# Kernel optimization log

Measured on AMD Instinct MI355X. Metric: run time of the kernel, lower is better.

The kernel has to match this reference:

```python
import jax, jax.numpy as jnp
import numpy as np

B, C, C2, E = 4, 1024, 1024, 1024
D = 1024          # context_size (d_q = d_kv)
NH = 16           # module's n_heads arg -> actual head_dim after the quirky view
G = D // NH       # effective number of head groups = 64


def setup_inputs() -> dict:
    key = jax.random.key(0)
    ks = jax.random.split(key, 6)
    s = 0.02
    return {
        "x1": jax.random.normal(ks[0], (B, C, E), dtype=jnp.float32),
        "x2": jax.random.normal(ks[1], (B, C2, E), dtype=jnp.float32),
        "W_q": jax.random.normal(ks[2], (E, D), dtype=jnp.float32) * s,
        "W_k": jax.random.normal(ks[3], (E, D), dtype=jnp.float32) * s,
        "W_v": jax.random.normal(ks[4], (E, D), dtype=jnp.float32) * s,
        "W_o": jax.random.normal(ks[5], (D, D), dtype=jnp.float32) * s,
    }


def _split_heads(t):
    # (B, S, D) -> view (B, S, G, NH) -> transpose(1,2) -> (B, G, S, NH)
    b, s, _ = t.shape
    return jnp.transpose(t.reshape(b, s, G, NH), (0, 2, 1, 3))


def reference(x1, x2, W_q, W_k, W_v, W_o):
    Q = _split_heads(x1 @ W_q)   # (B, G, C, NH)
    K = _split_heads(x2 @ W_k)   # (B, G, C2, NH)
    V = _split_heads(x2 @ W_v)   # (B, G, C2, NH)
    scale = 1.0 / jnp.sqrt(jnp.asarray(NH, dtype=Q.dtype))
    scores = jnp.einsum("bgqh,bgkh->bgqk", Q, K) * scale  # (B, G, C, C2)
    w = jax.nn.softmax(scores, axis=-1)
    out = jnp.einsum("bgqk,bgkh->bgqh", w, V)             # (B, G, C, NH)
    out = jnp.transpose(out, (0, 2, 1, 3)).reshape(B, C, D)
    return out @ W_o  # dropout p=0 -> identity
```

## Files before the change

kernel.cpp:

```cpp
#include <hip/hip_runtime.h>


typedef _Float16 f16x8 __attribute__((ext_vector_type(8)));
typedef _Float16 f16x4 __attribute__((ext_vector_type(4)));
typedef _Float16 f16x2 __attribute__((ext_vector_type(2)));
typedef float    f32x4 __attribute__((ext_vector_type(4)));

#define GLOAD_LDS16(gp, lp)                                              \
    __builtin_amdgcn_global_load_lds(                                    \
        (const __attribute__((address_space(1))) void*)(gp),             \
        (__attribute__((address_space(3))) void*)(lp), 16, 0, 0)

static __device__ __forceinline__ f16x4 pack4(f32x4 p) {
    f16x2 a = __builtin_bit_cast(f16x2, __builtin_amdgcn_cvt_pkrtz(p[0], p[1]));
    f16x2 b = __builtin_bit_cast(f16x2, __builtin_amdgcn_cvt_pkrtz(p[2], p[3]));
    f16x4 r; r[0] = a[0]; r[1] = a[1]; r[2] = b[0]; r[3] = b[1];
    return r;
}

__global__ __launch_bounds__(256) void cvt2_kernel(const float* __restrict__ x1,
                                                   const float* __restrict__ x2,
                                                   _Float16* __restrict__ y1,
                                                   _Float16* __restrict__ y2) {
    int i = blockIdx.x * 256 + threadIdx.x;
    const float* x = (i < 1048576) ? x1 : x2;
    _Float16* y = (i < 1048576) ? y1 : y2;
    int j = i & 1048575;
    float4 v = ((const float4*)x)[j];
    f16x4 h = { (_Float16)v.x, (_Float16)v.y, (_Float16)v.z, (_Float16)v.w };
    ((f16x4*)y)[j] = h;
}

__global__ __launch_bounds__(256) void transpose_cvt4_kernel(
        const float* __restrict__ W0, const float* __restrict__ W1,
        const float* __restrict__ W2, const float* __restrict__ W3,
        _Float16* __restrict__ T0, _Float16* __restrict__ T1,
        _Float16* __restrict__ T2, _Float16* __restrict__ T3) {
    int z = blockIdx.z;
    const float* W = (z == 0) ? W0 : (z == 1) ? W1 : (z == 2) ? W2 : W3;
    _Float16* WT = (z == 0) ? T0 : (z == 1) ? T1 : (z == 2) ? T2 : T3;
    __shared__ float tile[32][33];
    int tx = threadIdx.x, ty = threadIdx.y;
    int c0 = blockIdx.x * 32, r0 = blockIdx.y * 32;
#pragma unroll
    for (int i = 0; i < 32; i += 8)
        tile[ty + i][tx] = W[(r0 + ty + i) * 1024 + (c0 + tx)];
    __syncthreads();
#pragma unroll
    for (int i = 0; i < 32; i += 8)
        WT[(c0 + ty + i) * 1024 + (r0 + tx)] = (_Float16)tile[tx][ty + i];
}

template <bool OUTF32>
static __device__ __forceinline__ void gemm_body(const _Float16* __restrict__ A,
                                                 const _Float16* __restrict__ BT,
                                                 void* __restrict__ Cout,
                                                 _Float16* As, _Float16* Bs) {
    const int tid = threadIdx.x, lane = tid & 63, wave = tid >> 6;
    const int wm = wave >> 1, wn = wave & 1;
    const int col = lane & 15, quad = lane >> 4;
    const int m0 = blockIdx.y * 128, n0 = blockIdx.x * 128;

    f32x4 acc[4][4];
#pragma unroll
    for (int i = 0; i < 4; i++)
#pragma unroll
        for (int j = 0; j < 4; j++) acc[i][j] = (f32x4){0.f, 0.f, 0.f, 0.f};

    const int srow = wave * 8 + (lane >> 3);
    const int sch = (lane & 7) * 8;
    const _Float16* Ag = A + (size_t)(m0 + srow) * 1024 + sch;
    const _Float16* Bg = BT + (size_t)(n0 + srow) * 1024 + sch;
    _Float16* Asl = As + wave * 512;
    _Float16* Bsl = Bs + wave * 512;

    for (int kt = 0; kt < 16; kt++) {
        __syncthreads();
#pragma unroll
        for (int c = 0; c < 4; c++) {
            GLOAD_LDS16(Ag + (size_t)(c * 32) * 1024 + kt * 64, Asl + c * 2048);
            GLOAD_LDS16(Bg + (size_t)(c * 32) * 1024 + kt * 64, Bsl + c * 2048);
        }
        __syncthreads();
#pragma unroll
        for (int ki = 0; ki < 2; ki++) {
            f16x8 af[4], bf[4];
#pragma unroll
            for (int i = 0; i < 4; i++)
                af[i] = *(const f16x8*)(As + (wm * 64 + i * 16 + col) * 64 + ki * 32 + quad * 8);
#pragma unroll
            for (int j = 0; j < 4; j++)
                bf[j] = *(const f16x8*)(Bs + (wn * 64 + j * 16 + col) * 64 + ki * 32 + quad * 8);
#pragma unroll
            for (int i = 0; i < 4; i++)
#pragma unroll
                for (int j = 0; j < 4; j++)
                    acc[i][j] = __builtin_amdgcn_mfma_f32_16x16x32_f16(af[i], bf[j], acc[i][j], 0, 0, 0);
        }
    }

#pragma unroll
    for (int i = 0; i < 4; i++)
#pragma unroll
        for (int ii = 0; ii < 4; ii++) {
            int row = m0 + wm * 64 + i * 16 + quad * 4 + ii;
#pragma unroll
            for (int j = 0; j < 4; j++) {
                int cc = n0 + wn * 64 + j * 16 + col;
                if (OUTF32) ((float*)Cout)[(size_t)row * 1024 + cc] = acc[i][j][ii];
                else ((_Float16*)Cout)[(size_t)row * 1024 + cc] = (_Float16)acc[i][j][ii];
            }
        }
}

__global__ __launch_bounds__(256, 3) void gemm_qkv_kernel(
        const _Float16* __restrict__ x1h, const _Float16* __restrict__ x2h,
        const _Float16* __restrict__ WqT, const _Float16* __restrict__ WkT,
        const _Float16* __restrict__ WvT,
        _Float16* __restrict__ Qh, _Float16* __restrict__ Kh, _Float16* __restrict__ Vh) {
    __shared__ _Float16 As[128 * 64], Bs[128 * 64];
    int z = blockIdx.z;
    const _Float16* A = (z == 0) ? x1h : x2h;
    const _Float16* BT = (z == 0) ? WqT : (z == 1) ? WkT : WvT;
    _Float16* C = (z == 0) ? Qh : (z == 1) ? Kh : Vh;
    gemm_body<false>(A, BT, (void*)C, As, Bs);
}

__global__ __launch_bounds__(256, 3) void gemm_wo_kernel(const _Float16* __restrict__ Ah,
                                                         const _Float16* __restrict__ WoT,
                                                         float* __restrict__ out) {
    __shared__ _Float16 As[128 * 64], Bs[128 * 64];
    gemm_body<true>(Ah, WoT, (void*)out, As, Bs);
}

__global__ __launch_bounds__(512, 4) void attn_kernel(const _Float16* __restrict__ Qh,
                                                      const _Float16* __restrict__ Kh,
                                                      const _Float16* __restrict__ Vh,
                                                      _Float16* __restrict__ Ah) {
    int pair = blockIdx.y;
    int b = pair >> 6, g = pair & 63;
    extern __shared__ _Float16 smem[];
    _Float16* Ks = smem;
    _Float16* Vts = smem + 16384;

    const _Float16* Kg = Kh + (size_t)(b * 1024) * 1024 + g * 16;
    const _Float16* Vg = Vh + (size_t)(b * 1024) * 1024 + g * 16;
    int tid = threadIdx.x;
#pragma unroll
    for (int it = 0; it < 4; it++) {
        int row = it * 256 + (tid >> 1);
        int part = (tid & 1) * 8;
        *(uint4*)(Ks + row * 16 + part) = *(const uint4*)(Kg + (size_t)row * 1024 + part);
    }
#pragma unroll
    for (int it = 0; it < 4; it++) {
        int row = it * 256 + (tid >> 1);
        int part = (tid & 1) * 8;
        f16x8 v = *(const f16x8*)(Vg + (size_t)row * 1024 + part);
#pragma unroll
        for (int j = 0; j < 8; j++) {
            int h = part + j;
            Vts[h * 1024 + ((row + 68 * h) & 1023)] = v[j];
        }
    }
    __syncthreads();

    int lane = tid & 63, wave = tid >> 6;
    int col = lane & 15, quad = lane >> 4;
    int q0 = blockIdx.x * 512 + wave * 64;

    f16x4 qf[4];
    const _Float16* qb = Qh + (size_t)(b * 1024 + q0 + col) * 1024 + g * 16 + quad * 4;
#pragma unroll
    for (int qg = 0; qg < 4; qg++) {
        f16x4 t = *(const f16x4*)(qb + (size_t)qg * 16 * 1024);
#pragma unroll
        for (int j = 0; j < 4; j++) qf[qg][j] = (_Float16)((float)t[j] * 0.360673760f);
    }

    f32x4 O[4], L[4];
#pragma unroll
    for (int qg = 0; qg < 4; qg++) {
        O[qg] = (f32x4){0.f, 0.f, 0.f, 0.f};
        L[qg] = (f32x4){0.f, 0.f, 0.f, 0.f};
    }
    const f16x4 ones = {(_Float16)1.f, (_Float16)1.f, (_Float16)1.f, (_Float16)1.f};
    const int vrot = 68 * col;
    const f32x4 zero = {0.f, 0.f, 0.f, 0.f};

#pragma unroll 2
    for (int t = 0; t < 32; t++) {
        f16x4 ak0 = *(const f16x4*)(Ks + (t * 32 + col) * 16 + quad * 4);
        f16x4 ak1 = *(const f16x4*)(Ks + (t * 32 + 16 + col) * 16 + quad * 4);
        f16x4 av0 = *(const f16x4*)(Vts + col * 1024 + ((t * 32 + quad * 4 + vrot) & 1023));
        f16x4 av1 = *(const f16x4*)(Vts + col * 1024 + ((t * 32 + 16 + quad * 4 + vrot) & 1023));
#pragma unroll
        for (int qg = 0; qg < 4; qg++) {
            f32x4 s0 = __builtin_amdgcn_mfma_f32_16x16x16f16(ak0, qf[qg], zero, 0, 0, 0);
            f32x4 s1 = __builtin_amdgcn_mfma_f32_16x16x16f16(ak1, qf[qg], zero, 0, 0, 0);
            f32x4 p0, p1;
#pragma unroll
            for (int i = 0; i < 4; i++) p0[i] = __builtin_amdgcn_exp2f(s0[i]);
#pragma unroll
            for (int i = 0; i < 4; i++) p1[i] = __builtin_amdgcn_exp2f(s1[i]);
            f16x4 pb0 = pack4(p0), pb1 = pack4(p1);
            O[qg] = __builtin_amdgcn_mfma_f32_16x16x16f16(av0, pb0, O[qg], 0, 0, 0);
            O[qg] = __builtin_amdgcn_mfma_f32_16x16x16f16(av1, pb1, O[qg], 0, 0, 0);
            L[qg] = __builtin_amdgcn_mfma_f32_16x16x16f16(ones, pb0, L[qg], 0, 0, 0);
            L[qg] = __builtin_amdgcn_mfma_f32_16x16x16f16(ones, pb1, L[qg], 0, 0, 0);
        }
    }

    _Float16* ob = Ah + (size_t)(b * 1024 + q0 + col) * 1024 + g * 16 + quad * 4;
#pragma unroll
    for (int qg = 0; qg < 4; qg++) {
        float rl = 1.0f / L[qg][0];
        f16x4 ov;
#pragma unroll
        for (int i = 0; i < 4; i++) ov[i] = (_Float16)(O[qg][i] * rl);
        *(f16x4*)(ob + (size_t)qg * 16 * 1024) = ov;
    }
}

extern "C" void kernel_launch(void* const* d_in, const int* in_sizes, int n_in,
                              void* d_out, int out_size, void* d_ws, size_t ws_size,
                              hipStream_t stream) {
    const float* x1 = (const float*)d_in[0];
    const float* x2 = (const float*)d_in[1];
    const float* Wq = (const float*)d_in[2];
    const float* Wk = (const float*)d_in[3];
    const float* Wv = (const float*)d_in[4];
    const float* Wo = (const float*)d_in[5];

    char* ws = (char*)d_ws;
    const size_t MB = 1u << 20;
    if (ws_size < 56 * MB) return;

    _Float16* x1h = (_Float16*)(ws + 0 * MB);
    _Float16* x2h = (_Float16*)(ws + 8 * MB);
    _Float16* WqT = (_Float16*)(ws + 16 * MB);
    _Float16* WkT = (_Float16*)(ws + 18 * MB);
    _Float16* WvT = (_Float16*)(ws + 20 * MB);
    _Float16* WoT = (_Float16*)(ws + 22 * MB);
    _Float16* Qh  = (_Float16*)(ws + 24 * MB);
    _Float16* Kh  = (_Float16*)(ws + 32 * MB);
    _Float16* Vh  = (_Float16*)(ws + 40 * MB);
    _Float16* Ah  = (_Float16*)(ws + 48 * MB);

    cvt2_kernel<<<8192, 256, 0, stream>>>(x1, x2, x1h, x2h);

    transpose_cvt4_kernel<<<dim3(32, 32, 4), dim3(32, 8), 0, stream>>>(
        Wq, Wk, Wv, Wo, WqT, WkT, WvT, WoT);

    gemm_qkv_kernel<<<dim3(8, 32, 3), 256, 0, stream>>>(x1h, x2h, WqT, WkT, WvT, Qh, Kh, Vh);

    attn_kernel<<<dim3(2, 256), 512, 65536, stream>>>(Qh, Kh, Vh, Ah);

    gemm_wo_kernel<<<dim3(8, 32), 256, 0, stream>>>(Ah, WoT, (float*)d_out);
}
```

Measured before the change: 216.0 us.

## Chunk K/V staging into halves and use 16x16x32 MFMA for PV

Result: faster. 210.4 us (-2.6%).

```diff
diff --git a/kernel.cpp b/kernel.cpp
--- a/kernel.cpp
+++ b/kernel.cpp
@@ -11,10 +11,14 @@
         (const __attribute__((address_space(1))) void*)(gp),             \
         (__attribute__((address_space(3))) void*)(lp), 16, 0, 0)
 
-static __device__ __forceinline__ f16x4 pack4(f32x4 p) {
-    f16x2 a = __builtin_bit_cast(f16x2, __builtin_amdgcn_cvt_pkrtz(p[0], p[1]));
-    f16x2 b = __builtin_bit_cast(f16x2, __builtin_amdgcn_cvt_pkrtz(p[2], p[3]));
-    f16x4 r; r[0] = a[0]; r[1] = a[1]; r[2] = b[0]; r[3] = b[1];
+static __device__ __forceinline__ f16x8 pack8(f32x4 p0, f32x4 p1) {
+    f16x2 a = __builtin_bit_cast(f16x2, __builtin_amdgcn_cvt_pkrtz(p0[0], p0[1]));
+    f16x2 b = __builtin_bit_cast(f16x2, __builtin_amdgcn_cvt_pkrtz(p0[2], p0[3]));
+    f16x2 c = __builtin_bit_cast(f16x2, __builtin_amdgcn_cvt_pkrtz(p1[0], p1[1]));
+    f16x2 d = __builtin_bit_cast(f16x2, __builtin_amdgcn_cvt_pkrtz(p1[2], p1[3]));
+    f16x8 r;
+    r[0] = a[0]; r[1] = a[1]; r[2] = b[0]; r[3] = b[1];
+    r[4] = c[0]; r[5] = c[1]; r[6] = d[0]; r[7] = d[1];
     return r;
 }
 
@@ -133,87 +137,91 @@
     gemm_body<true>(Ah, WoT, (void*)out, As, Bs);
 }
 
-__global__ __launch_bounds__(512, 4) void attn_kernel(const _Float16* __restrict__ Qh,
+__global__ __launch_bounds__(512, 8) void attn_kernel(const _Float16* __restrict__ Qh,
                                                       const _Float16* __restrict__ Kh,
                                                       const _Float16* __restrict__ Vh,
                                                       _Float16* __restrict__ Ah) {
     int pair = blockIdx.y;
     int b = pair >> 6, g = pair & 63;
-    extern __shared__ _Float16 smem[];
-    _Float16* Ks = smem;
-    _Float16* Vts = smem + 16384;
+    __shared__ _Float16 Ks[512 * 16];
+    __shared__ _Float16 Vts[16 * 512];
 
     const _Float16* Kg = Kh + (size_t)(b * 1024) * 1024 + g * 16;
     const _Float16* Vg = Vh + (size_t)(b * 1024) * 1024 + g * 16;
     int tid = threadIdx.x;
-#pragma unroll
-    for (int it = 0; it < 4; it++) {
-        int row = it * 256 + (tid >> 1);
-        int part = (tid & 1) * 8;
-        *(uint4*)(Ks + row * 16 + part) = *(const uint4*)(Kg + (size_t)row * 1024 + part);
-    }
-#pragma unroll
-    for (int it = 0; it < 4; it++) {
-        int row = it * 256 + (tid >> 1);
-        int part = (tid & 1) * 8;
-        f16x8 v = *(const f16x8*)(Vg + (size_t)row * 1024 + part);
-#pragma unroll
-        for (int j = 0; j < 8; j++) {
-            int h = part + j;
-            Vts[h * 1024 + ((row + 68 * h) & 1023)] = v[j];
-        }
-    }
-    __syncthreads();
-
     int lane = tid & 63, wave = tid >> 6;
     int col = lane & 15, quad = lane >> 4;
-    int q0 = blockIdx.x * 512 + wave * 64;
-
-    f16x4 qf[4];
+    int q0 = blockIdx.x * 256 + wave * 32;
+
+    f16x4 qf[2];
     const _Float16* qb = Qh + (size_t)(b * 1024 + q0 + col) * 1024 + g * 16 + quad * 4;
 #pragma unroll
-    for (int qg = 0; qg < 4; qg++) {
+    for (int qg = 0; qg < 2; qg++) {
         f16x4 t = *(const f16x4*)(qb + (size_t)qg * 16 * 1024);
 #pragma unroll
         for (int j = 0; j < 4; j++) qf[qg][j] = (_Float16)((float)t[j] * 0.360673760f);
     }
 
-    f32x4 O[4], L[4];
-#pragma unroll
-    for (int qg = 0; qg < 4; qg++) {
+    f32x4 O[2], L[2];
+#pragma unroll
+    for (int qg = 0; qg < 2; qg++) {
         O[qg] = (f32x4){0.f, 0.f, 0.f, 0.f};
         L[qg] = (f32x4){0.f, 0.f, 0.f, 0.f};
     }
-    const f16x4 ones = {(_Float16)1.f, (_Float16)1.f, (_Float16)1.f, (_Float16)1.f};
-    const int vrot = 68 * col;
+    f16x8 ones8;
+#pragma unroll
+    for (int j = 0; j < 8; j++) ones8[j] = (_Float16)1.f;
     const f32x4 zero = {0.f, 0.f, 0.f, 0.f};
-
-#pragma unroll 2
-    for (int t = 0; t < 32; t++) {
-        f16x4 ak0 = *(const f16x4*)(Ks + (t * 32 + col) * 16 + quad * 4);
-        f16x4 ak1 = *(const f16x4*)(Ks + (t * 32 + 16 + col) * 16 + quad * 4);
-        f16x4 av0 = *(const f16x4*)(Vts + col * 1024 + ((t * 32 + quad * 4 + vrot) & 1023));
-        f16x4 av1 = *(const f16x4*)(Vts + col * 1024 + ((t * 32 + 16 + quad * 4 + vrot) & 1023));
-#pragma unroll
-        for (int qg = 0; qg < 4; qg++) {
-            f32x4 s0 = __builtin_amdgcn_mfma_f32_16x16x16f16(ak0, qf[qg], zero, 0, 0, 0);
-            f32x4 s1 = __builtin_amdgcn_mfma_f32_16x16x16f16(ak1, qf[qg], zero, 0, 0, 0);
-            f32x4 p0, p1;
-#pragma unroll
-            for (int i = 0; i < 4; i++) p0[i] = __builtin_amdgcn_exp2f(s0[i]);
-#pragma unroll
-            for (int i = 0; i < 4; i++) p1[i] = __builtin_amdgcn_exp2f(s1[i]);
-            f16x4 pb0 = pack4(p0), pb1 = pack4(p1);
-            O[qg] = __builtin_amdgcn_mfma_f32_16x16x16f16(av0, pb0, O[qg], 0, 0, 0);
-            O[qg] = __builtin_amdgcn_mfma_f32_16x16x16f16(av1, pb1, O[qg], 0, 0, 0);
-            L[qg] = __builtin_amdgcn_mfma_f32_16x16x16f16(ones, pb0, L[qg], 0, 0, 0);
-            L[qg] = __builtin_amdgcn_mfma_f32_16x16x16f16(ones, pb1, L[qg], 0, 0, 0);
+    const int krow0 = (col >> 2) * 8 + (col & 3);
+    const int vrot = 72 * col;
+
+    for (int c = 0; c < 2; c++) {
+        if (c) __syncthreads();
+#pragma unroll
+        for (int it = 0; it < 2; it++) {
+            int row = it * 256 + (tid >> 1);
+            int part = (tid & 1) * 8;
+            *(uint4*)(Ks + row * 16 + part) =
+                *(const uint4*)(Kg + (size_t)(c * 512 + row) * 1024 + part);
+        }
+#pragma unroll
+        for (int it = 0; it < 2; it++) {
+            int row = it * 256 + (tid >> 1);
+            int part = (tid & 1) * 8;
+            f16x8 v = *(const f16x8*)(Vg + (size_t)(c * 512 + row) * 1024 + part);
+#pragma unroll
+            for (int j = 0; j < 8; j++) {
+                int h = part + j;
+                Vts[h * 512 + ((row + 72 * h) & 511)] = v[j];
+            }
+        }
+        __syncthreads();
+
+#pragma unroll 4
+        for (int t = 0; t < 16; t++) {
+            const _Float16* kb = Ks + (t * 32 + krow0) * 16 + quad * 4;
+            f16x4 ak0 = *(const f16x4*)(kb);
+            f16x4 ak1 = *(const f16x4*)(kb + 4 * 16);
+            f16x8 av = *(const f16x8*)(Vts + col * 512 + ((t * 32 + quad * 8 + vrot) & 511));
+#pragma unroll
+            for (int qg = 0; qg < 2; qg++) {
+                f32x4 s0 = __builtin_amdgcn_mfma_f32_16x16x16f16(ak0, qf[qg], zero, 0, 0, 0);
+                f32x4 s1 = __builtin_amdgcn_mfma_f32_16x16x16f16(ak1, qf[qg], zero, 0, 0, 0);
+                f32x4 p0, p1;
+#pragma unroll
+                for (int i = 0; i < 4; i++) p0[i] = __builtin_amdgcn_exp2f(s0[i]);
+#pragma unroll
+                for (int i = 0; i < 4; i++) p1[i] = __builtin_amdgcn_exp2f(s1[i]);
+                f16x8 pb = pack8(p0, p1);
+                O[qg] = __builtin_amdgcn_mfma_f32_16x16x32_f16(av, pb, O[qg], 0, 0, 0);
+                L[qg] = __builtin_amdgcn_mfma_f32_16x16x32_f16(ones8, pb, L[qg], 0, 0, 0);
+            }
         }
     }
 
     _Float16* ob = Ah + (size_t)(b * 1024 + q0 + col) * 1024 + g * 16 + quad * 4;
 #pragma unroll
-    for (int qg = 0; qg < 4; qg++) {
+    for (int qg = 0; qg < 2; qg++) {
         float rl = 1.0f / L[qg][0];
         f16x4 ov;
 #pragma unroll
@@ -254,7 +262,7 @@
 
     gemm_qkv_kernel<<<dim3(8, 32, 3), 256, 0, stream>>>(x1h, x2h, WqT, WkT, WvT, Qh, Kh, Vh);
 
-    attn_kernel<<<dim3(2, 256), 512, 65536, stream>>>(Qh, Kh, Vh, Ah);
+    attn_kernel<<<dim3(4, 256), 512, 0, stream>>>(Qh, Kh, Vh, Ah);
 
     gemm_wo_kernel<<<dim3(8, 32), 256, 0, stream>>>(Ah, WoT, (float*)d_out);
 }
```
